# Performance work log

Measured on AMD Instinct MI355X. Metric: run time of the kernel, lower is better.

## Reference

```python
import jax, jax.numpy as jnp
from jax import lax
import numpy as np

FSIZE = 5
NUM_FILTERS = 8


def setup_inputs() -> dict:
    key = jax.random.key(0)
    k1, k2, k3 = jax.random.split(key, 3)
    B, H, W = 8, 1024, 1024
    scale = 1.0 / (FSIZE * FSIZE)  # matches .normal_(0, 1/(fsize*fsize))
    return {
        "mosaick": jax.random.uniform(k1, (B, 1, H, W), dtype=jnp.float32),
        "sel_filts": jax.random.normal(k2, (NUM_FILTERS, FSIZE, FSIZE), dtype=jnp.float32) * scale,
        "green_filts": jax.random.normal(k3, (NUM_FILTERS, FSIZE, FSIZE), dtype=jnp.float32) * scale,
    }


def _conv_bank(x_padded, filts):
    # x_padded: [B,1,H+2p,W+2p], filts: [K,f,f] -> [B,K,H,W]
    return lax.conv_general_dilated(
        x_padded, filts[:, None, :, :], (1, 1), "VALID",
        dimension_numbers=("NCHW", "OIHW", "NCHW"))


def reference(mosaick, sel_filts, green_filts):
    # Space-variant learned demosaicking of the green channel:
    # per-pixel softmax over a bank of selection-filter responses picks a
    # convex combination of candidate green interpolations; known green
    # samples (GRBG: x%2 == y%2) are passed through from the mosaick.
    B, _, H, W = mosaick.shape
    p = FSIZE // 2
    padded = jnp.pad(mosaick, ((0, 0), (0, 0), (p, p), (p, p)), mode="edge")
    sel = _conv_bank(padded, sel_filts)        # [B,K,H,W] selection scores
    interp = _conv_bank(padded, green_filts)   # [B,K,H,W] green candidates
    w = jax.nn.softmax(sel, axis=1)            # per-pixel filter weights
    green_hat = jnp.sum(w * interp, axis=1, keepdims=True)  # [B,1,H,W]
    yy = jnp.arange(H)[:, None]
    xx = jnp.arange(W)[None, :]
    gmask = ((xx % 2) == (yy % 2)).astype(mosaick.dtype)  # GRBG green sites
    green = gmask * mosaick + (1.0 - gmask) * green_hat
    return green  # corresponds to output[:, 1:2, ...]
```

## Files before the change

kernel.cpp:

```cpp
#include <hip/hip_runtime.h>

#define HW_ (1024 * 1024)

typedef _Float16 half8 __attribute__((ext_vector_type(8)));
typedef float f32x16 __attribute__((ext_vector_type(16)));
typedef unsigned int uint;

__global__ __launch_bounds__(256, 2)
void demosaick_mfma2(const float* __restrict__ mosaick,
                     const float* __restrict__ sel_filts,
                     const float* __restrict__ green_filts,
                     float* __restrict__ out) {
    __shared__ __align__(16) _Float16 smem[3456];

    const int tid = threadIdx.x;
    const int b   = blockIdx.z;
    const int by0 = blockIdx.y * 16, bx0 = blockIdx.x * 64;
    const float* img = mosaick + (size_t)b * HW_;

    for (int idx = tid; idx < 1360; idx += 256) {
        int row = idx / 68, col = idx - row * 68;
        int gy = by0 - 2 + row; gy = gy < 0 ? 0 : (gy > 1023 ? 1023 : gy);
        int gx = bx0 - 2 + col; gx = gx < 0 ? 0 : (gx > 1023 ? 1023 : gx);
        smem[idx] = (_Float16)img[gy * 1024 + gx];
    }
    for (int idx = tid; idx < 2048; idx += 256) {
        int po = idx >> 10, m = (idx >> 5) & 31, kk = idx & 31;
        int pb = po, sdx = po ? 0 : 4;
        int dy = -1, dx = 0;
        if (kk < 16)           { int h = kk >> 3, j = kk & 7;
                                 dy = 2 * h + (j >> 2); dx = pb + (j & 3); }
        else if (kk < 18)      { dy = 4; dx = pb + (kk - 16); }
        else if (kk == 18)     { dy = 0; dx = sdx; }
        else if (kk == 19)     { dy = 1; dx = sdx; }
        else if (kk == 20)     { dy = 2; dx = sdx; }
        else if (kk >= 24 && kk < 26) { dy = 4; dx = pb + 2 + (kk - 24); }
        else if (kk == 26)     { dy = 3; dx = sdx; }
        else if (kk == 27)     { dy = 4; dx = sdx; }
        float v = 0.f;
        if (m < 16 && dy >= 0)
            v = ((m & 1) ? green_filts : sel_filts)[(m >> 1) * 25 + dy * 5 + dx];
        smem[1360 + idx] = (_Float16)v;
    }
    for (int idx = tid; idx < 32; idx += 256) smem[3408 + idx] = (_Float16)0.f;
    __syncthreads();

    const int lane = tid & 63, w = tid >> 6;
    const int n = lane & 31, h = lane >> 5;

    const half8 a0p0 = *(const half8*)&smem[1360 +        n * 32 + h * 8];
    const half8 a1p0 = *(const half8*)&smem[1360 +        n * 32 + 16 + h * 8];
    const half8 a0p1 = *(const half8*)&smem[1360 + 1024 + n * 32 + h * 8];
    const half8 a1p1 = *(const half8*)&smem[1360 + 1024 + n * 32 + 16 + h * 8];

    const uint* smw = (const uint*)smem;
    const unsigned short* sms = (const unsigned short*)smem;
    float* outp = out + (size_t)b * HW_;
    const float L2E = 1.44269504f;

    #pragma unroll
    for (int u = 0; u < 4; ++u) {
        const int r  = 4 * w + u;
        const int po = (u & 1) ^ 1;
        const int pb = po, sdx = po ? 0 : 4;
        const int e0 = (r + 2 * h) * 68 + 2 * n + po;
        const int e4 = (r + 4) * 68 + 2 * n + po;
        const int rs0 = h ? 3 : 0, rs1 = h ? 4 : 1;

        uint B0x = smw[(e0 + pb) >> 1];
        uint B0y = smw[(e0 + pb + 2) >> 1];
        uint B0z = smw[(e0 + 68 + pb) >> 1];
        uint B0w = smw[(e0 + 68 + pb + 2) >> 1];
        uint B1x = smw[(e4 + pb + 2 * h) >> 1];
        uint us0 = sms[(r + rs0) * 68 + 2 * n + po + sdx];
        uint us1 = sms[(r + rs1) * 68 + 2 * n + po + sdx];
        uint B1y = us0 | (us1 << 16);
        uint B1z = sms[h ? 3408 : ((r + 2) * 68 + 2 * n + po + sdx)];
        uint B1w = 0;

        union { uint u4[4]; half8 v; } b0c = {{B0x, B0y, B0z, B0w}};
        union { uint u4[4]; half8 v; } b1c = {{B1x, B1y, B1z, B1w}};

        f32x16 acc = {};
        acc = __builtin_amdgcn_mfma_f32_32x32x16_f16(po ? a0p1 : a0p0, b0c.v, acc, 0, 0, 0);
        acc = __builtin_amdgcn_mfma_f32_32x32x16_f16(po ? a1p1 : a1p0, b1c.v, acc, 0, 0, 0);

        float se = 0.f, eg = 0.f;
        #pragma unroll
        for (int rr = 0; rr < 8; rr += 2) {
            float e = __builtin_amdgcn_exp2f(acc[rr] * L2E);
            se += e;
            eg = fmaf(e, acc[rr + 1], eg);
        }
        eg += __shfl_xor(eg, 32);
        se += __shfl_xor(se, 32);
        float gh = eg * __builtin_amdgcn_rcpf(se);

        if (h == 1) {
            float pass = (float)(po ? b0c.v[0] : b0c.v[3]);
            float2 o;
            if (po) { o.x = pass; o.y = gh; }
            else    { o.x = gh;   o.y = pass; }
            *(float2*)(outp + (size_t)(by0 + r) * 1024 + bx0 + 2 * n) = o;
        }
    }
}

extern "C" void kernel_launch(void* const* d_in, const int* in_sizes, int n_in,
                              void* d_out, int out_size, void* d_ws, size_t ws_size,
                              hipStream_t stream) {
    const float* mosaick     = (const float*)d_in[0];
    const float* sel_filts   = (const float*)d_in[1];
    const float* green_filts = (const float*)d_in[2];
    float* out = (float*)d_out;
    const int B = in_sizes[0] / HW_;
    dim3 grid(1024 / 64, 1024 / 16, B);
    dim3 block(256, 1, 1);
    hipLaunchKernelGGL(demosaick_mfma2, grid, block, 0, stream,
                       mosaick, sel_filts, green_filts, out);
}
```

Baseline: 111.9 us.

## Precompute fp16 filter table in separate kernel and remap rows to drop shuffles

A small pre-kernel now builds the fp16 MFMA A-operand filter table once in workspace, so each main block no longer rebuilds it in shared memory. That shrinks LDS from about 6.9KB to 2.8KB and removes per-block filter address arithmetic. The filter row ordering is also remapped so each lane's 16 accumulator entries hold complete sel/green pairs, removing the cross-half shuffles at the cost of twice the exp work per lane. A fallback kernel is kept for when no workspace is available, and the extra launch adds a small fixed cost.

```diff
diff --git a/kernel.cpp b/kernel.cpp
--- a/kernel.cpp
+++ b/kernel.cpp
@@ -6,12 +6,42 @@
 typedef float f32x16 __attribute__((ext_vector_type(16)));
 typedef unsigned int uint;
 
+
+__device__ __forceinline__ void tap_from_kk(int po, int kk, int& dy, int& dx) {
+    const int pb = po, sdx = po ? 0 : 4;
+    dy = -1; dx = 0;
+    if (kk < 16)           { int h = kk >> 3, j = kk & 7;
+                             dy = 2 * h + (j >> 2); dx = pb + (j & 3); }
+    else if (kk < 18)      { dy = 4; dx = pb + (kk - 16); }
+    else if (kk == 18)     { dy = 0; dx = sdx; }
+    else if (kk == 19)     { dy = 1; dx = sdx; }
+    else if (kk == 20)     { dy = 2; dx = sdx; }
+    else if (kk >= 24 && kk < 26) { dy = 4; dx = pb + 2 + (kk - 24); }
+    else if (kk == 26)     { dy = 3; dx = sdx; }
+    else if (kk == 27)     { dy = 4; dx = sdx; }
+}
+
+__global__ void build_filter_table(const float* __restrict__ sel_filts,
+                                   const float* __restrict__ green_filts,
+                                   _Float16* __restrict__ tbl) {
+    int idx = blockIdx.x * 256 + threadIdx.x;
+    int po = idx >> 10, m = (idx >> 5) & 31, kk = idx & 31;
+    int dy, dx;
+    tap_from_kk(po, kk, dy, dx);
+    float v = 0.f;
+    if (dy >= 0) {
+        int t = m & 3;
+        int p = 2 * ((m >> 2) >> 1) + (t >> 1);
+        v = ((t & 1) ? green_filts : sel_filts)[p * 25 + dy * 5 + dx];
+    }
+    tbl[idx] = (_Float16)v;
+}
+
 __global__ __launch_bounds__(256, 2)
-void demosaick_mfma2(const float* __restrict__ mosaick,
-                     const float* __restrict__ sel_filts,
-                     const float* __restrict__ green_filts,
-                     float* __restrict__ out) {
-    __shared__ __align__(16) _Float16 smem[3456];
+void demosaick_main(const float* __restrict__ mosaick,
+                    const _Float16* __restrict__ tbl,
+                    float* __restrict__ out) {
+    __shared__ __align__(16) _Float16 smem[1392];
 
     const int tid = threadIdx.x;
     const int b   = blockIdx.z;
@@ -24,22 +54,96 @@
         int gx = bx0 - 2 + col; gx = gx < 0 ? 0 : (gx > 1023 ? 1023 : gx);
         smem[idx] = (_Float16)img[gy * 1024 + gx];
     }
+    if (tid < 32) smem[1360 + tid] = (_Float16)0.f;
+    __syncthreads();
+
+    const int lane = tid & 63, w = tid >> 6;
+    const int n = lane & 31, h = lane >> 5;
+
+    const half8* t8 = (const half8*)tbl;
+    const half8 a0p0 = t8[      n * 4 + h];
+    const half8 a1p0 = t8[      n * 4 + 2 + h];
+    const half8 a0p1 = t8[128 + n * 4 + h];
+    const half8 a1p1 = t8[128 + n * 4 + 2 + h];
+
+    const uint* smw = (const uint*)smem;
+    const unsigned short* sms = (const unsigned short*)smem;
+    float* outp = out + (size_t)b * HW_;
+    const float L2E = 1.44269504f;
+
+    #pragma unroll
+    for (int u = 0; u < 4; ++u) {
+        const int r  = 4 * w + u;
+        const int po = (u & 1) ^ 1;
+        const int pb = po, sdx = po ? 0 : 4;
+        const int e0 = (r + 2 * h) * 68 + 2 * n + po;
+        const int e4 = (r + 4) * 68 + 2 * n + po;
+        const int rs0 = h ? 3 : 0, rs1 = h ? 4 : 1;
+
+        uint B0x = smw[(e0 + pb) >> 1];
+        uint B0y = smw[(e0 + pb + 2) >> 1];
+        uint B0z = smw[(e0 + 68 + pb) >> 1];
+        uint B0w = smw[(e0 + 68 + pb + 2) >> 1];
+        uint B1x = smw[(e4 + pb + 2 * h) >> 1];
+        uint us0 = sms[(r + rs0) * 68 + 2 * n + po + sdx];
+        uint us1 = sms[(r + rs1) * 68 + 2 * n + po + sdx];
+        uint B1y = us0 | (us1 << 16);
+        uint B1z = sms[h ? 1360 : ((r + 2) * 68 + 2 * n + po + sdx)];
+        uint B1w = 0;
+
+        union { uint u4[4]; half8 v; } b0c = {{B0x, B0y, B0z, B0w}};
+        union { uint u4[4]; half8 v; } b1c = {{B1x, B1y, B1z, B1w}};
+
+        f32x16 acc = {};
+        acc = __builtin_amdgcn_mfma_f32_32x32x16_f16(po ? a0p1 : a0p0, b0c.v, acc, 0, 0, 0);
+        acc = __builtin_amdgcn_mfma_f32_32x32x16_f16(po ? a1p1 : a1p0, b1c.v, acc, 0, 0, 0);
+
+        float se = 0.f, eg = 0.f;
+        #pragma unroll
+        for (int rr = 0; rr < 16; rr += 2) {
+            float e = __builtin_amdgcn_exp2f(acc[rr] * L2E);
+            se += e;
+            eg = fmaf(e, acc[rr + 1], eg);
+        }
+        float gh = eg * __builtin_amdgcn_rcpf(se);
+
+        if (h == 1) {
+            float pass = (float)(po ? b0c.v[0] : b0c.v[3]);
+            float2 o;
+            if (po) { o.x = pass; o.y = gh; }
+            else    { o.x = gh;   o.y = pass; }
+            *(float2*)(outp + (size_t)(by0 + r) * 1024 + bx0 + 2 * n) = o;
+        }
+    }
+}
+
+__global__ __launch_bounds__(256, 2)
+void demosaick_fallback(const float* __restrict__ mosaick,
+                        const float* __restrict__ sel_filts,
+                        const float* __restrict__ green_filts,
+                        float* __restrict__ out) {
+    __shared__ __align__(16) _Float16 smem[3456];
+    const int tid = threadIdx.x;
+    const int b   = blockIdx.z;
+    const int by0 = blockIdx.y * 16, bx0 = blockIdx.x * 64;
+    const float* img = mosaick + (size_t)b * HW_;
+
+    for (int idx = tid; idx < 1360; idx += 256) {
+        int row = idx / 68, col = idx - row * 68;
+        int gy = by0 - 2 + row; gy = gy < 0 ? 0 : (gy > 1023 ? 1023 : gy);
+        int gx = bx0 - 2 + col; gx = gx < 0 ? 0 : (gx > 1023 ? 1023 : gx);
+        smem[idx] = (_Float16)img[gy * 1024 + gx];
+    }
     for (int idx = tid; idx < 2048; idx += 256) {
         int po = idx >> 10, m = (idx >> 5) & 31, kk = idx & 31;
-        int pb = po, sdx = po ? 0 : 4;
-        int dy = -1, dx = 0;
-        if (kk < 16)           { int h = kk >> 3, j = kk & 7;
-                                 dy = 2 * h + (j >> 2); dx = pb + (j & 3); }
-        else if (kk < 18)      { dy = 4; dx = pb + (kk - 16); }
-        else if (kk == 18)     { dy = 0; dx = sdx; }
-        else if (kk == 19)     { dy = 1; dx = sdx; }
-        else if (kk == 20)     { dy = 2; dx = sdx; }
-        else if (kk >= 24 && kk < 26) { dy = 4; dx = pb + 2 + (kk - 24); }
-        else if (kk == 26)     { dy = 3; dx = sdx; }
-        else if (kk == 27)     { dy = 4; dx = sdx; }
+        int dy, dx;
+        tap_from_kk(po, kk, dy, dx);
         float v = 0.f;
-        if (m < 16 && dy >= 0)
-            v = ((m & 1) ? green_filts : sel_filts)[(m >> 1) * 25 + dy * 5 + dx];
+        if (dy >= 0) {
+            int t = m & 3;
+            int p = 2 * ((m >> 2) >> 1) + (t >> 1);
+            v = ((t & 1) ? green_filts : sel_filts)[p * 25 + dy * 5 + dx];
+        }
         smem[1360 + idx] = (_Float16)v;
     }
     for (int idx = tid; idx < 32; idx += 256) smem[3408 + idx] = (_Float16)0.f;
@@ -47,7 +151,6 @@
 
     const int lane = tid & 63, w = tid >> 6;
     const int n = lane & 31, h = lane >> 5;
-
     const half8 a0p0 = *(const half8*)&smem[1360 +        n * 32 + h * 8];
     const half8 a1p0 = *(const half8*)&smem[1360 +        n * 32 + 16 + h * 8];
     const half8 a0p1 = *(const half8*)&smem[1360 + 1024 + n * 32 + h * 8];
@@ -87,13 +190,11 @@
 
         float se = 0.f, eg = 0.f;
         #pragma unroll
-        for (int rr = 0; rr < 8; rr += 2) {
+        for (int rr = 0; rr < 16; rr += 2) {
             float e = __builtin_amdgcn_exp2f(acc[rr] * L2E);
             se += e;
             eg = fmaf(e, acc[rr + 1], eg);
         }
-        eg += __shfl_xor(eg, 32);
-        se += __shfl_xor(se, 32);
         float gh = eg * __builtin_amdgcn_rcpf(se);
 
         if (h == 1) {
@@ -116,6 +217,15 @@
     const int B = in_sizes[0] / HW_;
     dim3 grid(1024 / 64, 1024 / 16, B);
     dim3 block(256, 1, 1);
-    hipLaunchKernelGGL(demosaick_mfma2, grid, block, 0, stream,
-                       mosaick, sel_filts, green_filts, out);
-}
+
+    if (ws_size >= 4096) {
+        _Float16* tbl = (_Float16*)d_ws;
+        hipLaunchKernelGGL(build_filter_table, dim3(8), dim3(256), 0, stream,
+                           sel_filts, green_filts, tbl);
+        hipLaunchKernelGGL(demosaick_main, grid, block, 0, stream,
+                           mosaick, tbl, out);
+    } else {
+        hipLaunchKernelGGL(demosaick_fallback, grid, block, 0, stream,
+                           mosaick, sel_filts, green_filts, out);
+    }
+}
```

Result: faster. 103.5 us (-7.5%).
